# Kernel tuning notes

Measured on AMD Instinct MI355X. Metric: run time of the kernel, lower is better.

The kernel has to match this reference:

```python
import jax, jax.numpy as jnp
import numpy as np

D_MODEL, D_STATE, D_CONV, EXPAND = 1024, 16, 4, 2
D_INNER = EXPAND * D_MODEL
DT_RANK = (D_MODEL + 15) // 16  # 64
B_SZ, SEQ = 2, 1024


def _mamba_dir(x, inW, convW, convB, xpW, dtW, dtB, Alog, Dp, outW):
    """Standard Mamba block forward. x: [B, L, d_model]."""
    Bsz, L, _ = x.shape
    d_inner, d_state = Alog.shape
    dt_rank = xpW.shape[0] - 2 * d_state
    xz = jnp.einsum('bld,ed->ble', x, inW)            # [B, L, 2*d_inner]
    xi, z = jnp.split(xz, 2, axis=-1)
    # depthwise causal conv along L
    xc = jnp.swapaxes(xi, 1, 2)                       # [B, d_inner, L]
    xc = jax.lax.conv_general_dilated(
        xc, convW, window_strides=(1,),
        padding=[(convW.shape[-1] - 1, 0)],
        feature_group_count=d_inner)
    xc = xc + convB[None, :, None]
    u = jax.nn.silu(jnp.swapaxes(xc, 1, 2))           # [B, L, d_inner]
    x_dbl = jnp.einsum('bld,ed->ble', u, xpW)         # [B, L, dt_rank+2N]
    dt, Bm, Cm = jnp.split(x_dbl, [dt_rank, dt_rank + d_state], axis=-1)
    delta = jax.nn.softplus(jnp.einsum('blr,dr->bld', dt, dtW) + dtB)  # [B,L,d_inner]
    A = -jnp.exp(Alog)                                # [d_inner, d_state]

    def step(h, ins):
        d_t, B_t, C_t, u_t = ins                      # [B,D],[B,N],[B,N],[B,D]
        dA = jnp.exp(d_t[:, :, None] * A)             # [B, D, N]
        h = h * dA + (d_t * u_t)[:, :, None] * B_t[:, None, :]
        y_t = jnp.einsum('bdn,bn->bd', h, C_t)
        return h, y_t

    h0 = jnp.zeros((Bsz, d_inner, d_state), x.dtype)
    xs = (jnp.swapaxes(delta, 0, 1), jnp.swapaxes(Bm, 0, 1),
          jnp.swapaxes(Cm, 0, 1), jnp.swapaxes(u, 0, 1))
    _, ys = jax.lax.scan(step, h0, xs)
    y = jnp.swapaxes(ys, 0, 1)                        # [B, L, d_inner]
    y = y + u * Dp
    y = y * jax.nn.silu(z)
    return jnp.einsum('bld,od->blo', y, outW)         # [B, L, d_model]


def _make_params(key, suffix):
    ks = jax.random.split(key, 10)
    s = 0.02
    p = {
        'inW' + suffix: jax.random.normal(ks[0], (2 * D_INNER, D_MODEL), jnp.float32) * s,
        'convW' + suffix: jax.random.normal(ks[1], (D_INNER, 1, D_CONV), jnp.float32) * s,
        'convB' + suffix: jnp.zeros((D_INNER,), jnp.float32),
        'xpW' + suffix: jax.random.normal(ks[2], (DT_RANK + 2 * D_STATE, D_INNER), jnp.float32) * s,
        'dtW' + suffix: jax.random.normal(ks[3], (D_INNER, DT_RANK), jnp.float32) * s,
        'dtB' + suffix: jax.random.normal(ks[4], (D_INNER,), jnp.float32) * 0.1 - 4.0,
        'Alog' + suffix: jnp.log(1.0 + jax.random.uniform(ks[5], (D_INNER, D_STATE), jnp.float32) * 15.0),
        'Dp' + suffix: jnp.ones((D_INNER,), jnp.float32),
        'outW' + suffix: jax.random.normal(ks[6], (D_MODEL, D_INNER), jnp.float32) * s,
    }
    return p


def setup_inputs() -> dict:
    key = jax.random.key(0)
    kx, kf, kb = jax.random.split(key, 3)
    inp = {'x': jax.random.normal(kx, (B_SZ, SEQ, D_MODEL), jnp.float32)}
    inp.update(_make_params(kf, '_f'))
    inp.update(_make_params(kb, '_b'))
    return inp


def reference(x, inW_f, convW_f, convB_f, xpW_f, dtW_f, dtB_f, Alog_f, Dp_f, outW_f,
              inW_b, convW_b, convB_b, xpW_b, dtW_b, dtB_b, Alog_b, Dp_b, outW_b):
    y_fwd = _mamba_dir(x, inW_f, convW_f, convB_f, xpW_f, dtW_f, dtB_f, Alog_f, Dp_f, outW_f)
    xb = jnp.flip(x, axis=1)
    y_bwd = jnp.flip(_mamba_dir(xb, inW_b, convW_b, convB_b, xpW_b, dtW_b, dtB_b, Alog_b, Dp_b, outW_b), axis=1)
    return 0.5 * (y_fwd + y_bwd)
```

## Files before the change

kernel.cpp:

```cpp
#include <hip/hip_runtime.h>
#include <math.h>

#define B_SZ 2
#define SEQ  1024
#define DM   1024
#define DI   2048
#define NST  16
#define RNK  64
#define XPD  96
#define M_TOT (B_SZ*SEQ)
#define NC   64
#define LC   (SEQ/NC)
#define NCH  65536

typedef unsigned short ushort_t;
typedef __attribute__((ext_vector_type(8))) short short8;
typedef __attribute__((ext_vector_type(4))) float f32x4;

#if __has_builtin(__builtin_amdgcn_exp2f)
#define EXP2F __builtin_amdgcn_exp2f
#else
#define EXP2F exp2f
#endif
#define LOG2E 1.44269504f

__device__ __forceinline__ ushort_t f2bf(float f) {
    unsigned u = __float_as_uint(f);
    u += 0x7fff + ((u >> 16) & 1);
    return (ushort_t)(u >> 16);
}
__device__ __forceinline__ float bf2f(ushort_t v) {
    return __uint_as_float(((unsigned)v) << 16);
}

__global__ __launch_bounds__(256)
void convert_all(const float* __restrict__ x,
                 const float* __restrict__ inWf, const float* __restrict__ inWb,
                 const float* __restrict__ outWf, const float* __restrict__ outWb,
                 const float* __restrict__ xpWf, const float* __restrict__ xpWb,
                 ushort_t* __restrict__ xbf, ushort_t* __restrict__ inWcat,
                 ushort_t* __restrict__ outWcat, ushort_t* __restrict__ xpWcat)
{
    int bid = blockIdx.x;
    const float* src; ushort_t* dst; int rel; int strided = 0;
    if (bid < 2048)       { rel = bid;         src = x;     dst = xbf; }
    else if (bid < 6144)  { rel = bid - 2048;  src = inWf;  dst = inWcat; }
    else if (bid < 10240) { rel = bid - 6144;  src = inWb;  dst = inWcat + (size_t)2 * DI * DM; }
    else if (bid < 12288) { rel = bid - 10240; src = outWf; dst = outWcat;      strided = 1; }
    else if (bid < 14336) { rel = bid - 12288; src = outWb; dst = outWcat + DI; strided = 1; }
    else if (bid < 14528) { rel = bid - 14336; src = xpWf;  dst = xpWcat; }
    else                  { rel = bid - 14528; src = xpWb;  dst = xpWcat + (size_t)XPD * DI; }
    int i = rel * 256 + threadIdx.x;
    float4 v = ((const float4*)src)[i];
    ushort4 o;
    o.x = f2bf(v.x); o.y = f2bf(v.y); o.z = f2bf(v.z); o.w = f2bf(v.w);
    if (!strided) {
        ((ushort4*)dst)[i] = o;
    } else {
        int row = i >> 9;
        int c4  = (i - (row << 9)) << 2;
        *(ushort4*)(dst + (size_t)row * (2 * DI) + c4) = o;
    }
}

__device__ __forceinline__ void load_lds16(const ushort_t* g, ushort_t* l) {
    __builtin_amdgcn_global_load_lds(
        (const __attribute__((address_space(1))) void*)g,
        (__attribute__((address_space(3))) void*)l, 16, 0, 0);
}

#define GK  1024
#define GLD 8192
#define GNT 16

__device__ __forceinline__ void stageHalf(const ushort_t* g, int grow0, int kt,
                                          ushort_t* lds, int w8, int l8, int gch)
{
    const ushort_t* p = g + (size_t)(grow0 + w8 + l8) * GK + (size_t)kt * 64 + (gch << 3);
    load_lds16(p,                   lds + w8 * 64);
    load_lds16(p + (size_t)64 * GK, lds + (64 + w8) * 64);
}

__device__ __forceinline__ void rdA4(const ushort_t* buf, int rbase, int sw0, int sw1,
                                     short8 (&a)[4][2])
{
#pragma unroll
    for (int i = 0; i < 4; i++) {
        const ushort_t* p = buf + (size_t)(rbase + i * 16) * 64;
        a[i][0] = *(const short8*)(p + sw0);
        a[i][1] = *(const short8*)(p + sw1);
    }
}
__device__ __forceinline__ void rdB2(const ushort_t* buf, int rbase, int sw0, int sw1,
                                     short8 (&bb)[2][2])
{
#pragma unroll
    for (int j = 0; j < 2; j++) {
        const ushort_t* p = buf + (size_t)(rbase + j * 16) * 64;
        bb[j][0] = *(const short8*)(p + sw0);
        bb[j][1] = *(const short8*)(p + sw1);
    }
}
__device__ __forceinline__ void mm16(const short8 (&a)[4][2], const short8 (&bb)[2][2],
                                     f32x4 (&acc)[4][2])
{
#pragma unroll
    for (int i = 0; i < 4; i++)
#pragma unroll
        for (int j = 0; j < 2; j++) {
            acc[i][j] = __builtin_amdgcn_mfma_f32_16x16x32_bf16(a[i][0], bb[j][0], acc[i][j], 0, 0, 0);
            acc[i][j] = __builtin_amdgcn_mfma_f32_16x16x32_bf16(a[i][1], bb[j][1], acc[i][j], 0, 0, 0);
        }
}

#define BAR()        __builtin_amdgcn_s_barrier()
#define SCHEDB()     __builtin_amdgcn_sched_barrier(0)
#define PRIO1()      __builtin_amdgcn_s_setprio(1)
#define PRIO0()      __builtin_amdgcn_s_setprio(0)
#define WAIT_LGKM0() asm volatile("s_waitcnt lgkmcnt(0)" ::: "memory")
#define WAIT_VM6()   asm volatile("s_waitcnt vmcnt(6)"  ::: "memory")
#define WAIT_VM0()   asm volatile("s_waitcnt vmcnt(0)"  ::: "memory")

__global__ __launch_bounds__(512, 2)
void gemm256_bf16(const ushort_t* __restrict__ A, const ushort_t* __restrict__ W,
                  ushort_t* __restrict__ D)
{
    __shared__ __align__(16) ushort_t As[2][256 * 64];
    __shared__ __align__(16) ushort_t Bs[2][256 * 64];

    const int t_   = threadIdx.x;
    const int lane = t_ & 63;
    const int wave = t_ >> 6;
    const int wrq  = wave >> 2;
    const int wcq  = wave & 3;
    const int lm   = lane & 15;
    const int w8   = wave << 3;
    const int l8   = lane >> 3;
    const int gch  = (lane & 7) ^ l8;
    const int sw0  = (((lane >> 4)    ) ^ (lane & 7)) << 3;
    const int sw1  = (((lane >> 4) + 4) ^ (lane & 7)) << 3;

    const int m0 = blockIdx.y * 256;
    const int n0 = blockIdx.x * 256;

    const int rA0 = wrq * 64 + lm, rA1 = 128 + rA0;
    const int rB0 = wcq * 32 + lm, rB1 = 128 + rB0;

    f32x4 acc[2][2][4][2] = {};
    short8 a[4][2], b0[2][2], b1[2][2];

    stageHalf(A, m0,       0, &As[0][0],        w8, l8, gch);
    stageHalf(A, m0 + 128, 0, &As[0][128 * 64], w8, l8, gch);
    stageHalf(W, n0,       0, &Bs[0][0],        w8, l8, gch);
    stageHalf(W, n0 + 128, 0, &Bs[0][128 * 64], w8, l8, gch);
    stageHalf(A, m0,       1, &As[1][0],        w8, l8, gch);
    stageHalf(W, n0,       1, &Bs[1][0],        w8, l8, gch);
    stageHalf(W, n0 + 128, 1, &Bs[1][128 * 64], w8, l8, gch);
    WAIT_VM6();
    BAR();

#pragma unroll
    for (int t = 0; t < GNT; ++t) {
        const int b = t & 1;
        const ushort_t* Ab = &As[b][0];
        const ushort_t* Bb = &Bs[b][0];
        ushort_t* Abw = &As[b][0];
        ushort_t* Bbw = &Bs[b][0];
        ushort_t* Aow = &As[b ^ 1][0];

        rdA4(Ab, rA0, sw0, sw1, a);
        rdB2(Bb, rB0, sw0, sw1, b0);
        if (t + 1 < GNT) stageHalf(A, m0 + 128, t + 1, Aow + 128 * 64, w8, l8, gch);
        SCHEDB(); BAR(); WAIT_LGKM0(); SCHEDB();
        PRIO1(); mm16(a, b0, acc[0][0]); PRIO0();
        SCHEDB(); BAR();

        rdB2(Bb, rB1, sw0, sw1, b1);
        if (t + 2 < GNT) stageHalf(A, m0, t + 2, Abw, w8, l8, gch);
        SCHEDB(); BAR(); WAIT_LGKM0(); SCHEDB();
        PRIO1(); mm16(a, b1, acc[0][1]); PRIO0();
        SCHEDB(); BAR();

        rdA4(Ab, rA1, sw0, sw1, a);
        if (t + 2 < GNT) stageHalf(W, n0, t + 2, Bbw, w8, l8, gch);
        SCHEDB(); BAR(); WAIT_LGKM0(); SCHEDB();
        PRIO1(); mm16(a, b1, acc[1][1]); PRIO0();
        SCHEDB(); BAR();

        if (t + 2 < GNT) stageHalf(W, n0 + 128, t + 2, Bbw + 128 * 64, w8, l8, gch);
        SCHEDB(); BAR();
        PRIO1(); mm16(a, b0, acc[1][0]); PRIO0();
        SCHEDB();
        if (t < GNT - 2) { WAIT_VM6(); } else { WAIT_VM0(); }
        BAR();
    }

#pragma unroll
    for (int ih = 0; ih < 2; ih++)
#pragma unroll
        for (int i = 0; i < 4; i++)
#pragma unroll
            for (int r = 0; r < 4; r++) {
                int m = m0 + ih * 128 + wrq * 64 + i * 16 + ((lane >> 4) << 2) + r;
#pragma unroll
                for (int jh = 0; jh < 2; jh++)
#pragma unroll
                    for (int j = 0; j < 2; j++) {
                        int n = n0 + jh * 128 + wcq * 32 + j * 16 + lm;
                        D[(size_t)m * GLD + n] = f2bf(acc[ih][jh][i][j][r]);
                    }
            }
}

template<bool OUT_BF16>
__global__ __launch_bounds__(256)
void gemm_gll(const ushort_t* __restrict__ A, const ushort_t* __restrict__ W,
              void* __restrict__ D, int M, int N, int K, int kLen, int ldD)
{
    __shared__ __align__(16) ushort_t As[128 * 64];
    __shared__ __align__(16) ushort_t Ws[128 * 64];
    const int t    = threadIdx.x;
    const int lane = t & 63;
    const int wave = t >> 6;
    const int wr   = (wave >> 1) * 64;
    const int wc   = (wave & 1) * 64;

    const int m0 = blockIdx.y * 128;
    const int n0 = blockIdx.x * 128;
    const int kStart = blockIdx.z * kLen;

    const int srow   = lane >> 3;
    const int gchunk = (lane & 7) ^ srow;

    f32x4 acc[4][4] = {};

    for (int k0 = kStart; k0 < kStart + kLen; k0 += 64) {
#pragma unroll
        for (int it = 0; it < 4; it++) {
            const int rb = wave * 32 + it * 8;
            load_lds16(A + (size_t)(m0 + rb + srow) * K + k0 + gchunk * 8,
                       As + rb * 64);
            load_lds16(W + (size_t)(n0 + rb + srow) * K + k0 + gchunk * 8,
                       Ws + rb * 64);
        }
        __syncthreads();
#pragma unroll
        for (int kk = 0; kk < 2; kk++) {
            const int kc = kk * 4 + (lane >> 4);
            short8 af[4], bf[4];
#pragma unroll
            for (int i = 0; i < 4; i++) {
                int r = wr + i * 16 + (lane & 15);
                af[i] = *(const short8*)(As + r * 64 + ((kc ^ (r & 7)) << 3));
            }
#pragma unroll
            for (int j = 0; j < 4; j++) {
                int r = wc + j * 16 + (lane & 15);
                bf[j] = *(const short8*)(Ws + r * 64 + ((kc ^ (r & 7)) << 3));
            }
#pragma unroll
            for (int i = 0; i < 4; i++)
#pragma unroll
                for (int j = 0; j < 4; j++)
                    acc[i][j] = __builtin_amdgcn_mfma_f32_16x16x32_bf16(
                        af[i], bf[j], acc[i][j], 0, 0, 0);
        }
        __syncthreads();
    }

    if (OUT_BF16) {
        ushort_t* Dp = (ushort_t*)D;
#pragma unroll
        for (int i = 0; i < 4; i++)
#pragma unroll
            for (int r = 0; r < 4; r++) {
                int m = m0 + wr + i * 16 + ((lane >> 4) << 2) + r;
#pragma unroll
                for (int j = 0; j < 4; j++) {
                    int n = n0 + wc + j * 16 + (lane & 15);
                    Dp[(size_t)m * ldD + n] = f2bf(acc[i][j][r]);
                }
            }
    } else {
        float* Dp = (float*)D + (size_t)blockIdx.z * M * ldD;
#pragma unroll
        for (int i = 0; i < 4; i++)
#pragma unroll
            for (int r = 0; r < 4; r++) {
                int m = m0 + wr + i * 16 + ((lane >> 4) << 2) + r;
#pragma unroll
                for (int j = 0; j < 4; j++) {
                    int n = n0 + wc + j * 16 + (lane & 15);
                    Dp[(size_t)m * ldD + n] = acc[i][j][r];
                }
            }
    }
}

__global__ __launch_bounds__(256)
void reduce4(const float* __restrict__ P, float* __restrict__ out)
{
    int i = blockIdx.x * 256 + threadIdx.x;
    const size_t S = (size_t)M_TOT * DM / 4;
    float4 a = ((const float4*)P)[i];
    float4 b = ((const float4*)P)[i + S];
    float4 c = ((const float4*)P)[i + 2 * S];
    float4 d = ((const float4*)P)[i + 3 * S];
    float4 o;
    o.x = 0.5f * (a.x + b.x + c.x + d.x);
    o.y = 0.5f * (a.y + b.y + c.y + d.y);
    o.z = 0.5f * (a.z + b.z + c.z + d.z);
    o.w = 0.5f * (a.w + b.w + c.w + d.w);
    ((float4*)out)[i] = o;
}

#define LDSP 72

__global__ __launch_bounds__(256)
void gemm2_splitk2(const ushort_t* __restrict__ ubf, const ushort_t* __restrict__ xpWcat,
                   float* __restrict__ P)
{
    const int dir = blockIdx.z >> 3;
    const int kz  = blockIdx.z & 7;
    const ushort_t* A = ubf + (size_t)dir * M_TOT * DI;
    const ushort_t* W = xpWcat + (size_t)dir * XPD * DI;
    const int K = DI, N = XPD;

    __shared__ __align__(16) ushort_t As[64 * LDSP];
    __shared__ __align__(16) ushort_t Ws[64 * LDSP];
    const int t    = threadIdx.x;
    const int lane = t & 63;
    const int wave = t >> 6;
    const int wr   = (wave >> 1) * 32;
    const int wc   = (wave & 1) * 32;

    f32x4 acc[2][2] = {};

    const int m0 = blockIdx.y * 64;
    const int n0 = blockIdx.x * 64;
    const int kStart = kz * (DI / 8);
    const int srow = t >> 3;
    const int scol = (t & 7) << 3;

    for (int k0 = kStart; k0 < kStart + DI / 8; k0 += 64) {
        {
            int r = srow;
            short8 v = *(const short8*)(A + (size_t)(m0 + r) * K + k0 + scol);
            *(short8*)(&As[r * LDSP + scol]) = v;
            int r2 = 32 + srow;
            short8 v2 = *(const short8*)(A + (size_t)(m0 + r2) * K + k0 + scol);
            *(short8*)(&As[r2 * LDSP + scol]) = v2;
            int wn = n0 + r;
            short8 wv = {};
            if (wn < N) wv = *(const short8*)(W + (size_t)wn * K + k0 + scol);
            *(short8*)(&Ws[r * LDSP + scol]) = wv;
            int wn2 = n0 + r2;
            short8 wv2 = {};
            if (wn2 < N) wv2 = *(const short8*)(W + (size_t)wn2 * K + k0 + scol);
            *(short8*)(&Ws[r2 * LDSP + scol]) = wv2;
        }
        __syncthreads();
#pragma unroll
        for (int kk = 0; kk < 2; kk++) {
            const int kcol = kk * 32 + ((lane >> 4) << 3);
            short8 af[2], bfr[2];
#pragma unroll
            for (int i = 0; i < 2; i++)
                af[i] = *(const short8*)(&As[(wr + i * 16 + (lane & 15)) * LDSP + kcol]);
#pragma unroll
            for (int j = 0; j < 2; j++)
                bfr[j] = *(const short8*)(&Ws[(wc + j * 16 + (lane & 15)) * LDSP + kcol]);
#pragma unroll
            for (int i = 0; i < 2; i++)
#pragma unroll
                for (int j = 0; j < 2; j++)
                    acc[i][j] = __builtin_amdgcn_mfma_f32_16x16x32_bf16(
                        af[i], bfr[j], acc[i][j], 0, 0, 0);
        }
        __syncthreads();
    }

    float* Pz = P + ((size_t)dir * 8 + kz) * M_TOT * XPD;
#pragma unroll
    for (int i = 0; i < 2; i++)
#pragma unroll
        for (int r = 0; r < 4; r++) {
            int m = m0 + wr + i * 16 + ((lane >> 4) << 2) + r;
#pragma unroll
            for (int j = 0; j < 2; j++) {
                int n = n0 + wc + j * 16 + (lane & 15);
                if (n < N) Pz[(size_t)m * XPD + n] = acc[i][j][r];
            }
        }
}

__global__ __launch_bounds__(256)
void xdbl_reduce2(const float* __restrict__ P, float* __restrict__ xdbl)
{
    int bid = blockIdx.x;
    int dir = bid >= 192;
    int i = (bid - dir * 192) * 256 + threadIdx.x;
    const size_t S = (size_t)M_TOT * XPD / 4;
    const float4* Pd = (const float4*)(P + (size_t)dir * 8 * M_TOT * XPD);
    float4 s = Pd[i];
#pragma unroll
    for (int z = 1; z < 8; z++) {
        float4 v = Pd[i + z * S];
        s.x += v.x; s.y += v.y; s.z += v.z; s.w += v.w;
    }
    ((float4*)(xdbl + (size_t)dir * M_TOT * XPD))[i] = s;
}

__global__ __launch_bounds__(256)
void delta_gemm2(const float* __restrict__ xdbl,
                 const float* __restrict__ dtWf, const float* __restrict__ dtWb,
                 const float* __restrict__ dtBf, const float* __restrict__ dtBb,
                 ushort_t* __restrict__ deltab)
{
    const int dir = blockIdx.z;
    const float* xd  = xdbl + (size_t)dir * M_TOT * XPD;
    const float* dtW = dir ? dtWb : dtWf;
    const float* dtB = dir ? dtBb : dtBf;
    ushort_t* delta  = deltab + (size_t)dir * M_TOT * DI;

    __shared__ __align__(16) ushort_t As[64 * LDSP];
    __shared__ __align__(16) ushort_t Ws[64 * LDSP];
    const int t    = threadIdx.x;
    const int lane = t & 63;
    const int wave = t >> 6;
    const int wr   = (wave >> 1) * 32;
    const int wc   = (wave & 1) * 32;

    const int m0 = blockIdx.y * 64;
    const int n0 = blockIdx.x * 64;
    const int srow = t >> 2;
    const int scol = (t & 3) << 4;

    {
        const float* ap = xd  + (size_t)(m0 + srow) * XPD + scol;
        const float* wp = dtW + (size_t)(n0 + srow) * RNK + scol;
        float4 a[4], w[4];
#pragma unroll
        for (int q = 0; q < 4; q++) { a[q] = ((const float4*)ap)[q]; w[q] = ((const float4*)wp)[q]; }
        __align__(16) ushort_t at[16], wt[16];
#pragma unroll
        for (int q = 0; q < 16; q++) {
            at[q] = f2bf(((const float*)a)[q]);
            wt[q] = f2bf(((const float*)w)[q]);
        }
        *(short8*)(&As[srow * LDSP + scol])     = *(const short8*)(at);
        *(short8*)(&As[srow * LDSP + scol + 8]) = *(const short8*)(at + 8);
        *(short8*)(&Ws[srow * LDSP + scol])     = *(const short8*)(wt);
        *(short8*)(&Ws[srow * LDSP + scol + 8]) = *(const short8*)(wt + 8);
    }
    __syncthreads();

    f32x4 acc[2][2] = {};
#pragma unroll
    for (int kk = 0; kk < 2; kk++) {
        const int kcol = kk * 32 + ((lane >> 4) << 3);
        short8 af[2], bfr[2];
#pragma unroll
        for (int i = 0; i < 2; i++)
            af[i] = *(const short8*)(&As[(wr + i * 16 + (lane & 15)) * LDSP + kcol]);
#pragma unroll
        for (int j = 0; j < 2; j++)
            bfr[j] = *(const short8*)(&Ws[(wc + j * 16 + (lane & 15)) * LDSP + kcol]);
#pragma unroll
        for (int i = 0; i < 2; i++)
#pragma unroll
            for (int j = 0; j < 2; j++)
                acc[i][j] = __builtin_amdgcn_mfma_f32_16x16x32_bf16(
                    af[i], bfr[j], acc[i][j], 0, 0, 0);
    }

#pragma unroll
    for (int j = 0; j < 2; j++) {
        int n = n0 + wc + j * 16 + (lane & 15);
        float bn = dtB[n];
#pragma unroll
        for (int i = 0; i < 2; i++) {
#pragma unroll
            for (int r = 0; r < 4; r++) {
                int m = m0 + wr + i * 16 + ((lane >> 4) << 2) + r;
                float v = acc[i][j][r] + bn;
                float sp = (v > 20.f) ? v : log1pf(__expf(v));
                delta[(size_t)m * DI + n] = f2bf(sp);
            }
        }
    }
}

__global__ __launch_bounds__(256)
void conv_silu2(const ushort_t* __restrict__ xzall,
                const float* __restrict__ convWf, const float* __restrict__ convWb,
                const float* __restrict__ convBf, const float* __restrict__ convBb,
                ushort_t* __restrict__ ubf)
{
    int bid = blockIdx.x;
    int dir = bid >> 12;
    int idx = (bid & 4095) * 256 + threadIdx.x;
    const float* convW = dir ? convWb : convWf;
    const float* convB = dir ? convBb : convBf;
    int di  = (idx & (DI / 4 - 1)) << 2;
    int m   = idx >> 9;
    int b   = m >> 10, l = m & (SEQ - 1);
    const ushort_t* xb = xzall + (size_t)b * SEQ * (4 * DI) + dir * (2 * DI) + di;

    float wv[4][4];
#pragma unroll
    for (int c = 0; c < 4; c++) {
        float4 w = *(const float4*)(convW + (di + c) * 4);
        wv[c][0] = w.x; wv[c][1] = w.y; wv[c][2] = w.z; wv[c][3] = w.w;
    }
    float4 cb = *(const float4*)(convB + di);
    float acc[4] = {cb.x, cb.y, cb.z, cb.w};
#pragma unroll
    for (int j = 0; j < 4; j++) {
        int srcl = dir ? (l + 3 - j) : (l - 3 + j);
        if ((unsigned)srcl < SEQ) {
            ushort4 xv = *(const ushort4*)(xb + (size_t)srcl * (4 * DI));
            acc[0] += wv[0][j] * bf2f(xv.x);
            acc[1] += wv[1][j] * bf2f(xv.y);
            acc[2] += wv[2][j] * bf2f(xv.z);
            acc[3] += wv[3][j] * bf2f(xv.w);
        }
    }
    ushort4 o;
    o.x = f2bf(acc[0] / (1.f + __expf(-acc[0])));
    o.y = f2bf(acc[1] / (1.f + __expf(-acc[1])));
    o.z = f2bf(acc[2] / (1.f + __expf(-acc[2])));
    o.w = f2bf(acc[3] / (1.f + __expf(-acc[3])));
    *(ushort4*)(ubf + (size_t)dir * M_TOT * DI + (size_t)m * DI + di) = o;
}

__global__ __launch_bounds__(256)
void scan_pass1_2(const ushort_t* __restrict__ deltab, const ushort_t* __restrict__ ubf,
                  const float* __restrict__ xdbl,
                  const float* __restrict__ Alogf, const float* __restrict__ Alogb,
                  ushort_t* __restrict__ Sb, float* __restrict__ SD)
{
    int tid = threadIdx.x, lane = tid & 63, wv = tid >> 6;
    int blk = blockIdx.x;
    int dir = blk >> 10;
    blk &= 1023;
    int dg = blk & 7;
    int bc = blk >> 3;
    int c  = bc & (NC - 1);
    int b  = bc >> 6;
    int d  = (dg * 4 + wv) * 64 + lane;
    int t0 = dir ? (SEQ - 1 - c * LC) : (c * LC);
    int rs = dir ? -1 : 1;

    const float* Alog = dir ? Alogb : Alogf;
    const ushort_t* dl_p = deltab + (size_t)dir * M_TOT * DI;
    const ushort_t* u_p  = ubf    + (size_t)dir * M_TOT * DI;
    const float*    xd   = xdbl   + (size_t)dir * M_TOT * XPD;
    ushort_t* Sbd = Sb + (size_t)dir * NC * NCH;
    float* SDd = SD + (size_t)dir * NC * B_SZ * DI;

    float ac2[NST];
#pragma unroll
    for (int q = 0; q < 4; q++) {
        float4 al = *(const float4*)(Alog + (size_t)d * NST + q * 4);
        ac2[q * 4 + 0] = -__expf(al.x) * LOG2E;
        ac2[q * 4 + 1] = -__expf(al.y) * LOG2E;
        ac2[q * 4 + 2] = -__expf(al.z) * LOG2E;
        ac2[q * 4 + 3] = -__expf(al.w) * LOG2E;
    }
    float h[NST];
#pragma unroll
    for (int n = 0; n < NST; n++) h[n] = 0.f;
    float sumD = 0.f;

#pragma unroll 4
    for (int l = 0; l < LC; l++) {
        int t = t0 + rs * l;
        size_t row = (size_t)b * SEQ + t;
        float dl = bf2f(dl_p[row * DI + d]);
        float uv = bf2f(u_p[row * DI + d]);
        const float* xr = xd + row * XPD + RNK;
        float4 Bv[4];
#pragma unroll
        for (int q = 0; q < 4; q++) Bv[q] = *(const float4*)(xr + q * 4);
        float dlu = dl * uv;
        sumD += dl;
#pragma unroll
        for (int n = 0; n < NST; n++) {
            float dA = EXP2F(dl * ac2[n]);
            h[n] = h[n] * dA + dlu * ((const float*)Bv)[n];
        }
    }

    size_t o = (size_t)c * NCH + ((size_t)b * DI + d) * NST;
#pragma unroll
    for (int q = 0; q < 4; q++) {
        ushort4 pk;
        pk.x = f2bf(h[q * 4 + 0]);
        pk.y = f2bf(h[q * 4 + 1]);
        pk.z = f2bf(h[q * 4 + 2]);
        pk.w = f2bf(h[q * 4 + 3]);
        *(ushort4*)(Sbd + o + q * 4) = pk;
    }
    SDd[(size_t)c * (B_SZ * DI) + b * DI + d] = sumD;
}

__global__ __launch_bounds__(256)
void scan_combine2(ushort_t* __restrict__ Sb, const float* __restrict__ SD,
                   const float* __restrict__ Alogf, const float* __restrict__ Alogb)
{
    int gid = blockIdx.x * 256 + threadIdx.x;
    int dir = gid >= NCH;
    int i = gid - dir * NCH;
    int n = i & 15;
    int d = (i >> 4) & (DI - 1);
    int b = i >> 15;
    const float* Alog = dir ? Alogb : Alogf;
    ushort_t* Sbd = Sb + (size_t)dir * NC * NCH;
    const float* SDd = SD + (size_t)dir * NC * B_SZ * DI;
    float ac2 = -__expf(Alog[(size_t)d * NST + n]) * LOG2E;
    float h = 0.f;
#pragma unroll
    for (int c = 0; c < NC; c++) {
        float s = bf2f(Sbd[(size_t)c * NCH + i]);
        float p = EXP2F(ac2 * SDd[(size_t)c * (B_SZ * DI) + b * DI + d]);
        Sbd[(size_t)c * NCH + i] = f2bf(h);
        h = s + p * h;
    }
}

__global__ __launch_bounds__(256)
void scan_pass2_2(const ushort_t* __restrict__ deltab, const ushort_t* __restrict__ ubf,
                  const float* __restrict__ xdbl, const ushort_t* __restrict__ xzall,
                  const float* __restrict__ Alogf, const float* __restrict__ Alogb,
                  const float* __restrict__ Dpf, const float* __restrict__ Dpb,
                  const ushort_t* __restrict__ Hinit, ushort_t* __restrict__ ybf)
{
    int tid = threadIdx.x, lane = tid & 63, wv = tid >> 6;
    int blk = blockIdx.x;
    int dir = blk >> 10;
    blk &= 1023;
    int dg = blk & 7;
    int bc = blk >> 3;
    int c  = bc & (NC - 1);
    int b  = bc >> 6;
    int d  = (dg * 4 + wv) * 64 + lane;
    int t0 = dir ? (SEQ - 1 - c * LC) : (c * LC);
    int rs = dir ? -1 : 1;

    const float* Alog = dir ? Alogb : Alogf;
    const float* Dpp  = dir ? Dpb : Dpf;
    const ushort_t* dl_p = deltab + (size_t)dir * M_TOT * DI;
    const ushort_t* u_p  = ubf    + (size_t)dir * M_TOT * DI;
    const float*    xd   = xdbl   + (size_t)dir * M_TOT * XPD;
    const ushort_t* Hin  = Hinit  + (size_t)dir * NC * NCH;

    float ac2[NST];
#pragma unroll
    for (int q = 0; q < 4; q++) {
        float4 al = *(const float4*)(Alog + (size_t)d * NST + q * 4);
        ac2[q * 4 + 0] = -__expf(al.x) * LOG2E;
        ac2[q * 4 + 1] = -__expf(al.y) * LOG2E;
        ac2[q * 4 + 2] = -__expf(al.z) * LOG2E;
        ac2[q * 4 + 3] = -__expf(al.w) * LOG2E;
    }
    float dp = Dpp[d];
    float h[NST];
    {
        size_t o = (size_t)c * NCH + ((size_t)b * DI + d) * NST;
#pragma unroll
        for (int q = 0; q < 4; q++) {
            ushort4 hv = *(const ushort4*)(Hin + o + q * 4);
            h[q*4]   = bf2f(hv.x);
            h[q*4+1] = bf2f(hv.y);
            h[q*4+2] = bf2f(hv.z);
            h[q*4+3] = bf2f(hv.w);
        }
    }

#pragma unroll 4
    for (int l = 0; l < LC; l++) {
        int t = t0 + rs * l;
        size_t row = (size_t)b * SEQ + t;
        float dl = bf2f(dl_p[row * DI + d]);
        float uv = bf2f(u_p[row * DI + d]);
        const float* xr = xd + row * XPD + RNK;
        float4 Bv[4], Cv[4];
#pragma unroll
        for (int q = 0; q < 4; q++) {
            Bv[q] = *(const float4*)(xr + q * 4);
            Cv[q] = *(const float4*)(xr + NST + q * 4);
        }
        float dlu = dl * uv;
        float y = 0.f;
#pragma unroll
        for (int n = 0; n < NST; n++) {
            float dA = EXP2F(dl * ac2[n]);
            h[n] = h[n] * dA + dlu * ((const float*)Bv)[n];
            y += h[n] * ((const float*)Cv)[n];
        }
        float z = bf2f(xzall[row * (4 * DI) + dir * (2 * DI) + DI + d]);
        float yv = (y + uv * dp) * (z / (1.f + __expf(-z)));
        ybf[row * (2 * DI) + dir * DI + d] = f2bf(yv);
    }
}

extern "C" void kernel_launch(void* const* d_in, const int* in_sizes, int n_in,
                              void* d_out, int out_size, void* d_ws, size_t ws_size,
                              hipStream_t stream)
{
    char* wsb = (char*)d_ws;

    ushort_t* xzall  = (ushort_t*)wsb;
    ushort_t* ybf    = (ushort_t*)(wsb + 33554432);
    ushort_t* inWcat = (ushort_t*)(wsb + 50331648);
    ushort_t* outWcat= (ushort_t*)(wsb + 67108864);
    ushort_t* xbf    = (ushort_t*)(wsb + 75497472);
    ushort_t* xpWcat = (ushort_t*)(wsb + 79691776);
    ushort_t* ubf    = (ushort_t*)(wsb + 80478208);
    ushort_t* deltab = (ushort_t*)(wsb + 97255424);
    float*    xdbl   = (float*)(wsb + 114032640);

    ushort_t* Sb   = (ushort_t*)inWcat;
    float* SD    = (float*)xbf;
    float* part2 = (float*)deltab;
    float* part4 = (float*)xzall;

    float* out = (float*)d_out;
    dim3 blk(256);

    convert_all<<<14720, blk, 0, stream>>>(
        (const float*)d_in[0], (const float*)d_in[1], (const float*)d_in[10],
        (const float*)d_in[9], (const float*)d_in[18],
        (const float*)d_in[4], (const float*)d_in[13],
        xbf, inWcat, outWcat, xpWcat);

    gemm256_bf16<<<dim3(8192 / 256, M_TOT / 256), dim3(512), 0, stream>>>(
        xbf, inWcat, xzall);

    conv_silu2<<<8192, blk, 0, stream>>>(xzall,
        (const float*)d_in[2], (const float*)d_in[11],
        (const float*)d_in[3], (const float*)d_in[12], ubf);

    gemm2_splitk2<<<dim3(2, M_TOT / 64, 16), blk, 0, stream>>>(ubf, xpWcat, part2);

    xdbl_reduce2<<<384, blk, 0, stream>>>(part2, xdbl);

    delta_gemm2<<<dim3(DI / 64, M_TOT / 64, 2), blk, 0, stream>>>(
        xdbl, (const float*)d_in[5], (const float*)d_in[14],
        (const float*)d_in[6], (const float*)d_in[15], deltab);

    scan_pass1_2<<<2048, blk, 0, stream>>>(deltab, ubf, xdbl,
        (const float*)d_in[7], (const float*)d_in[16], Sb, SD);
    scan_combine2<<<2 * NCH / 256, blk, 0, stream>>>(Sb, SD,
        (const float*)d_in[7], (const float*)d_in[16]);
    scan_pass2_2<<<2048, blk, 0, stream>>>(deltab, ubf, xdbl, xzall,
        (const float*)d_in[7], (const float*)d_in[16],
        (const float*)d_in[8], (const float*)d_in[17], Sb, ybf);

    gemm_gll<false><<<dim3(DM / 128, M_TOT / 128, 4), blk, 0, stream>>>(
        ybf, outWcat, part4, M_TOT, DM, 2 * DI, DI / 2, DM);

    reduce4<<<(M_TOT * DM / 4) / 256, blk, 0, stream>>>(part4, out);
}
```

Baseline: 338.1 us.

## Split scan state dimension across wave halves to double scan parallelism

Both chunked scan passes now assign each channel to two lanes, each handling 8 of the 16 state entries, and launch twice as many blocks. In pass 2 the partial outputs are combined with a cross-half shuffle, and only one half does the gating and the store. The intent is more waves in flight and fewer registers per thread for the latency-bound recurrence. The cost is duplicated delta/u loads, half-wave coalescing (32 channels per wave), and idle lanes during the epilogue.

```diff
diff --git a/kernel.cpp b/kernel.cpp
--- a/kernel.cpp
+++ b/kernel.cpp
@@ -541,14 +541,15 @@
                   ushort_t* __restrict__ Sb, float* __restrict__ SD)
 {
     int tid = threadIdx.x, lane = tid & 63, wv = tid >> 6;
+    int l32 = lane & 31, hl = lane >> 5;
     int blk = blockIdx.x;
-    int dir = blk >> 10;
-    blk &= 1023;
-    int dg = blk & 7;
-    int bc = blk >> 3;
+    int dir = blk >> 11;
+    blk &= 2047;
+    int dg = blk & 15;
+    int bc = blk >> 4;
     int c  = bc & (NC - 1);
     int b  = bc >> 6;
-    int d  = (dg * 4 + wv) * 64 + lane;
+    int d  = (dg * 4 + wv) * 32 + l32;
     int t0 = dir ? (SEQ - 1 - c * LC) : (c * LC);
     int rs = dir ? -1 : 1;
 
@@ -559,18 +560,18 @@
     ushort_t* Sbd = Sb + (size_t)dir * NC * NCH;
     float* SDd = SD + (size_t)dir * NC * B_SZ * DI;
 
-    float ac2[NST];
-#pragma unroll
-    for (int q = 0; q < 4; q++) {
-        float4 al = *(const float4*)(Alog + (size_t)d * NST + q * 4);
+    float ac2[8];
+#pragma unroll
+    for (int q = 0; q < 2; q++) {
+        float4 al = *(const float4*)(Alog + (size_t)d * NST + hl * 8 + q * 4);
         ac2[q * 4 + 0] = -__expf(al.x) * LOG2E;
         ac2[q * 4 + 1] = -__expf(al.y) * LOG2E;
         ac2[q * 4 + 2] = -__expf(al.z) * LOG2E;
         ac2[q * 4 + 3] = -__expf(al.w) * LOG2E;
     }
-    float h[NST];
-#pragma unroll
-    for (int n = 0; n < NST; n++) h[n] = 0.f;
+    float h[8];
+#pragma unroll
+    for (int n = 0; n < 8; n++) h[n] = 0.f;
     float sumD = 0.f;
 
 #pragma unroll 4
@@ -579,22 +580,22 @@
         size_t row = (size_t)b * SEQ + t;
         float dl = bf2f(dl_p[row * DI + d]);
         float uv = bf2f(u_p[row * DI + d]);
-        const float* xr = xd + row * XPD + RNK;
-        float4 Bv[4];
-#pragma unroll
-        for (int q = 0; q < 4; q++) Bv[q] = *(const float4*)(xr + q * 4);
+        const float* xr = xd + row * XPD + RNK + hl * 8;
+        float4 Bv[2];
+#pragma unroll
+        for (int q = 0; q < 2; q++) Bv[q] = *(const float4*)(xr + q * 4);
         float dlu = dl * uv;
         sumD += dl;
 #pragma unroll
-        for (int n = 0; n < NST; n++) {
+        for (int n = 0; n < 8; n++) {
             float dA = EXP2F(dl * ac2[n]);
             h[n] = h[n] * dA + dlu * ((const float*)Bv)[n];
         }
     }
 
-    size_t o = (size_t)c * NCH + ((size_t)b * DI + d) * NST;
-#pragma unroll
-    for (int q = 0; q < 4; q++) {
+    size_t o = (size_t)c * NCH + ((size_t)b * DI + d) * NST + hl * 8;
+#pragma unroll
+    for (int q = 0; q < 2; q++) {
         ushort4 pk;
         pk.x = f2bf(h[q * 4 + 0]);
         pk.y = f2bf(h[q * 4 + 1]);
@@ -602,7 +603,8 @@
         pk.w = f2bf(h[q * 4 + 3]);
         *(ushort4*)(Sbd + o + q * 4) = pk;
     }
-    SDd[(size_t)c * (B_SZ * DI) + b * DI + d] = sumD;
+    if (hl == 0)
+        SDd[(size_t)c * (B_SZ * DI) + b * DI + d] = sumD;
 }
 
 __global__ __launch_bounds__(256)
@@ -637,14 +639,15 @@
                   const ushort_t* __restrict__ Hinit, ushort_t* __restrict__ ybf)
 {
     int tid = threadIdx.x, lane = tid & 63, wv = tid >> 6;
+    int l32 = lane & 31, hl = lane >> 5;
     int blk = blockIdx.x;
-    int dir = blk >> 10;
-    blk &= 1023;
-    int dg = blk & 7;
-    int bc = blk >> 3;
+    int dir = blk >> 11;
+    blk &= 2047;
+    int dg = blk & 15;
+    int bc = blk >> 4;
     int c  = bc & (NC - 1);
     int b  = bc >> 6;
-    int d  = (dg * 4 + wv) * 64 + lane;
+    int d  = (dg * 4 + wv) * 32 + l32;
     int t0 = dir ? (SEQ - 1 - c * LC) : (c * LC);
     int rs = dir ? -1 : 1;
 
@@ -655,21 +658,21 @@
     const float*    xd   = xdbl   + (size_t)dir * M_TOT * XPD;
     const ushort_t* Hin  = Hinit  + (size_t)dir * NC * NCH;
 
-    float ac2[NST];
-#pragma unroll
-    for (int q = 0; q < 4; q++) {
-        float4 al = *(const float4*)(Alog + (size_t)d * NST + q * 4);
+    float ac2[8];
+#pragma unroll
+    for (int q = 0; q < 2; q++) {
+        float4 al = *(const float4*)(Alog + (size_t)d * NST + hl * 8 + q * 4);
         ac2[q * 4 + 0] = -__expf(al.x) * LOG2E;
         ac2[q * 4 + 1] = -__expf(al.y) * LOG2E;
         ac2[q * 4 + 2] = -__expf(al.z) * LOG2E;
         ac2[q * 4 + 3] = -__expf(al.w) * LOG2E;
     }
     float dp = Dpp[d];
-    float h[NST];
+    float h[8];
     {
-        size_t o = (size_t)c * NCH + ((size_t)b * DI + d) * NST;
-#pragma unroll
-        for (int q = 0; q < 4; q++) {
+        size_t o = (size_t)c * NCH + ((size_t)b * DI + d) * NST + hl * 8;
+#pragma unroll
+        for (int q = 0; q < 2; q++) {
             ushort4 hv = *(const ushort4*)(Hin + o + q * 4);
             h[q*4]   = bf2f(hv.x);
             h[q*4+1] = bf2f(hv.y);
@@ -684,24 +687,28 @@
         size_t row = (size_t)b * SEQ + t;
         float dl = bf2f(dl_p[row * DI + d]);
         float uv = bf2f(u_p[row * DI + d]);
-        const float* xr = xd + row * XPD + RNK;
-        float4 Bv[4], Cv[4];
-#pragma unroll
-        for (int q = 0; q < 4; q++) {
-            Bv[q] = *(const float4*)(xr + q * 4);
-            Cv[q] = *(const float4*)(xr + NST + q * 4);
+        const float* xrB = xd + row * XPD + RNK + hl * 8;
+        const float* xrC = xrB + NST;
+        float4 Bv[2], Cv[2];
+#pragma unroll
+        for (int q = 0; q < 2; q++) {
+            Bv[q] = *(const float4*)(xrB + q * 4);
+            Cv[q] = *(const float4*)(xrC + q * 4);
         }
         float dlu = dl * uv;
         float y = 0.f;
 #pragma unroll
-        for (int n = 0; n < NST; n++) {
+        for (int n = 0; n < 8; n++) {
             float dA = EXP2F(dl * ac2[n]);
             h[n] = h[n] * dA + dlu * ((const float*)Bv)[n];
             y += h[n] * ((const float*)Cv)[n];
         }
-        float z = bf2f(xzall[row * (4 * DI) + dir * (2 * DI) + DI + d]);
-        float yv = (y + uv * dp) * (z / (1.f + __expf(-z)));
-        ybf[row * (2 * DI) + dir * DI + d] = f2bf(yv);
+        float ysum = y + __shfl_xor(y, 32);
+        if (hl == 0) {
+            float z = bf2f(xzall[row * (4 * DI) + dir * (2 * DI) + DI + d]);
+            float yv = (ysum + uv * dp) * (z / (1.f + __expf(-z)));
+            ybf[row * (2 * DI) + dir * DI + d] = f2bf(yv);
+        }
     }
 }
 
@@ -750,11 +757,11 @@
         xdbl, (const float*)d_in[5], (const float*)d_in[14],
         (const float*)d_in[6], (const float*)d_in[15], deltab);
 
-    scan_pass1_2<<<2048, blk, 0, stream>>>(deltab, ubf, xdbl,
+    scan_pass1_2<<<4096, blk, 0, stream>>>(deltab, ubf, xdbl,
         (const float*)d_in[7], (const float*)d_in[16], Sb, SD);
     scan_combine2<<<2 * NCH / 256, blk, 0, stream>>>(Sb, SD,
         (const float*)d_in[7], (const float*)d_in[16]);
-    scan_pass2_2<<<2048, blk, 0, stream>>>(deltab, ubf, xdbl, xzall,
+    scan_pass2_2<<<4096, blk, 0, stream>>>(deltab, ubf, xdbl, xzall,
         (const float*)d_in[7], (const float*)d_in[16],
         (const float*)d_in[8], (const float*)d_in[17], Sb, ybf);
 
```

Result: slower. 362.8 us (+7.3%).
